# Performance work log

Measured on AMD Instinct MI355X. Metric: run time of the kernel, lower is better.

The kernel has to match this reference:

```python
import jax, jax.numpy as jnp
import numpy as np

N, C, K, NUM_CLASS = 400000, 128, 128, 128


def setup_inputs() -> dict:
    key = jax.random.key(0)
    k1, k2, k3 = jax.random.split(key, 3)
    outputs = jax.random.normal(k1, (N, C), dtype=jnp.float32)
    labels = jax.random.randint(k2, (N,), 0, 2 * NUM_CLASS, dtype=jnp.int64 if jax.config.read('jax_enable_x64') else jnp.int32)
    global_logit = jax.random.normal(k3, (K, C), dtype=jnp.float32)
    return {"outputs": outputs, "labels": labels, "global_logit": global_logit, "k": NUM_CLASS}


def _pairwise_dist(x, protos):
    # Euclidean distance ||proto_j - x_i|| for all (i, j) without a [N,K,C] temp.
    x2 = jnp.sum(x * x, axis=1, keepdims=True)            # [N,1]
    p2 = jnp.sum(protos * protos, axis=1)[None, :]        # [1,K]
    d2 = x2 + p2 - 2.0 * (x @ protos.T)                   # [N,K]
    return jnp.sqrt(jnp.maximum(d2, 0.0))


def reference(outputs, labels, global_logit, k):
    # Rows with labels <= k-1 keep their label; rows with labels > k-1 get the
    # nearest-prototype index. Since the concatenated (labeled + pseudo-labeled)
    # set covers every row and CE-mean is order-invariant, we compute per-row
    # effective labels and a single mean cross-entropy.
    dists = _pairwise_dist(outputs, global_logit)          # [N,K]
    min_dist_labels = jnp.argmin(dists, axis=1)            # [N]
    is_labeled = labels <= (k - 1)
    labels_eff = jnp.where(is_labeled, labels, min_dist_labels)
    logp = jax.nn.log_softmax(outputs, axis=-1)            # [N,C]
    nll = -jnp.take_along_axis(logp, labels_eff[:, None].astype(jnp.int32), axis=1)[:, 0]
    return jnp.mean(nll)
```

## Files before the change

kernel.cpp:

```cpp
#include <hip/hip_runtime.h>
#include <hip/hip_bf16.h>


#define C_DIM 128
#define TILE_ROWS 32
#define NTHREADS 256
#define XSTRIDE 136

typedef __bf16 bf16x8 __attribute__((ext_vector_type(8)));
typedef unsigned short ushort8 __attribute__((ext_vector_type(8)));
typedef float f32x4 __attribute__((ext_vector_type(4)));

union FragU { ushort8 u; bf16x8 b; };

__device__ __forceinline__ unsigned short f2bf(float f) {
    unsigned int u = __float_as_uint(f);
    u += 0x7fffu + ((u >> 16) & 1u);
    return (unsigned short)(u >> 16);
}
__device__ __forceinline__ float bf2f(unsigned short h) {
    return __uint_as_float(((unsigned int)h) << 16);
}

extern "C" __global__ void __launch_bounds__(NTHREADS)
ploss_main(const float* __restrict__ x, const int* __restrict__ labels,
           const float* __restrict__ protos, const int* __restrict__ kptr,
           float* __restrict__ accum, int n_tiles)
{
    __shared__ __attribute__((aligned(16))) unsigned short x_lds[TILE_ROWS * XSTRIDE];
    __shared__ float lse_lds[TILE_ROWS];
    __shared__ float wmin_s[4][TILE_ROWS];
    __shared__ int   wmin_j[4][TILE_ROWS];

    const int tid  = threadIdx.x;
    const int lane = tid & 63;
    const int wave = tid >> 6;
    const int l15  = lane & 15;
    const int quad = lane >> 4;
    const int kk   = kptr[0];

    FragU bfrag[2][4];
    float p2h[2];
#pragma unroll
    for (int nt = 0; nt < 2; ++nt) {
        const int j = wave * 32 + nt * 16 + l15;
        const float* pr = protos + j * C_DIM;
        float s = 0.f;
#pragma unroll
        for (int c = 0; c < 32; c += 4) {
            float4 v = *(const float4*)(pr + quad * 32 + c);
            s += v.x*v.x + v.y*v.y + v.z*v.z + v.w*v.w;
        }
        s += __shfl_xor(s, 16);
        s += __shfl_xor(s, 32);
        p2h[nt] = 0.5f * s;
#pragma unroll
        for (int kt = 0; kt < 4; ++kt) {
            const float* pp = pr + kt * 32 + quad * 8;
            float4 v0 = *(const float4*)(pp);
            float4 v1 = *(const float4*)(pp + 4);
            FragU f;
            f.u[0]=f2bf(v0.x); f.u[1]=f2bf(v0.y); f.u[2]=f2bf(v0.z); f.u[3]=f2bf(v0.w);
            f.u[4]=f2bf(v1.x); f.u[5]=f2bf(v1.y); f.u[6]=f2bf(v1.z); f.u[7]=f2bf(v1.w);
            bfrag[nt][kt] = f;
        }
    }

    const int row_r = tid >> 3;
    const int row_q = tid & 7;

    float nll_acc = 0.f;

    for (int tile = blockIdx.x; tile < n_tiles; tile += gridDim.x) {
        const long long row0 = (long long)tile * TILE_ROWS;
        __syncthreads();

        const float* xr = x + (row0 + row_r) * C_DIM + row_q * 16;
        float4 a0 = *(const float4*)(xr);
        float4 a1 = *(const float4*)(xr + 4);
        float4 a2 = *(const float4*)(xr + 8);
        float4 a3 = *(const float4*)(xr + 12);

        float m = fmaxf(fmaxf(fmaxf(a0.x,a0.y),fmaxf(a0.z,a0.w)),
                        fmaxf(fmaxf(a1.x,a1.y),fmaxf(a1.z,a1.w)));
        m = fmaxf(m, fmaxf(fmaxf(fmaxf(a2.x,a2.y),fmaxf(a2.z,a2.w)),
                           fmaxf(fmaxf(a3.x,a3.y),fmaxf(a3.z,a3.w))));
        float s = __expf(a0.x-m)+__expf(a0.y-m)+__expf(a0.z-m)+__expf(a0.w-m)
                + __expf(a1.x-m)+__expf(a1.y-m)+__expf(a1.z-m)+__expf(a1.w-m)
                + __expf(a2.x-m)+__expf(a2.y-m)+__expf(a2.z-m)+__expf(a2.w-m)
                + __expf(a3.x-m)+__expf(a3.y-m)+__expf(a3.z-m)+__expf(a3.w-m);
#pragma unroll
        for (int mask = 1; mask <= 4; mask <<= 1) {
            float mo = __shfl_xor(m, mask);
            float so = __shfl_xor(s, mask);
            float nm = fmaxf(m, mo);
            s = s * __expf(m - nm) + so * __expf(mo - nm);
            m = nm;
        }
        if (row_q == 0) lse_lds[row_r] = m + __logf(s);

        FragU w0, w1;
        w0.u[0]=f2bf(a0.x); w0.u[1]=f2bf(a0.y); w0.u[2]=f2bf(a0.z); w0.u[3]=f2bf(a0.w);
        w0.u[4]=f2bf(a1.x); w0.u[5]=f2bf(a1.y); w0.u[6]=f2bf(a1.z); w0.u[7]=f2bf(a1.w);
        w1.u[0]=f2bf(a2.x); w1.u[1]=f2bf(a2.y); w1.u[2]=f2bf(a2.z); w1.u[3]=f2bf(a2.w);
        w1.u[4]=f2bf(a3.x); w1.u[5]=f2bf(a3.y); w1.u[6]=f2bf(a3.z); w1.u[7]=f2bf(a3.w);
        ushort8* dst = (ushort8*)&x_lds[row_r * XSTRIDE + row_q * 16];
        dst[0] = w0.u;
        dst[1] = w1.u;

        __syncthreads();

        f32x4 acc[2][2];
        f32x4 zero = {0.f, 0.f, 0.f, 0.f};
        acc[0][0]=zero; acc[0][1]=zero; acc[1][0]=zero; acc[1][1]=zero;
#pragma unroll
        for (int kt = 0; kt < 4; ++kt) {
#pragma unroll
            for (int mt = 0; mt < 2; ++mt) {
                FragU af;
                af.u = *(const ushort8*)&x_lds[(mt*16 + l15) * XSTRIDE + kt*32 + quad*8];
                acc[mt][0] = __builtin_amdgcn_mfma_f32_16x16x32_bf16(af.b, bfrag[0][kt].b, acc[mt][0], 0, 0, 0);
                acc[mt][1] = __builtin_amdgcn_mfma_f32_16x16x32_bf16(af.b, bfrag[1][kt].b, acc[mt][1], 0, 0, 0);
            }
        }

#pragma unroll
        for (int mt = 0; mt < 2; ++mt) {
#pragma unroll
            for (int reg = 0; reg < 4; ++reg) {
                float s0 = p2h[0] - acc[mt][0][reg];
                float s1 = p2h[1] - acc[mt][1][reg];
                int j0 = wave*32 + l15, j1 = j0 + 16;
                float sm; int jm;
                if (s1 < s0) { sm = s1; jm = j1; } else { sm = s0; jm = j0; }
#pragma unroll
                for (int mask = 1; mask <= 8; mask <<= 1) {
                    float so = __shfl_xor(sm, mask);
                    int   jo = __shfl_xor(jm, mask);
                    if (so < sm || (so == sm && jo < jm)) { sm = so; jm = jo; }
                }
                if (l15 == 0) {
                    int r = mt*16 + quad*4 + reg;
                    wmin_s[wave][r] = sm;
                    wmin_j[wave][r] = jm;
                }
            }
        }
        __syncthreads();

        if (tid < TILE_ROWS) {
            float bs = wmin_s[0][tid]; int bj = wmin_j[0][tid];
#pragma unroll
            for (int w = 1; w < 4; ++w) {
                float s2 = wmin_s[w][tid]; int j2 = wmin_j[w][tid];
                if (s2 < bs) { bs = s2; bj = j2; }
            }
            int lab = labels[row0 + tid];
            int eff = (lab <= kk - 1) ? lab : bj;
            float xv = bf2f(x_lds[tid * XSTRIDE + eff]);
            nll_acc += lse_lds[tid] - xv;
        }
    }

    if (wave == 0) {
        float v = nll_acc;
#pragma unroll
        for (int mask = 32; mask >= 1; mask >>= 1) v += __shfl_xor(v, mask);
        if (lane == 0) atomicAdd(accum, v);
    }
}

extern "C" __global__ void ploss_finalize(const float* __restrict__ accum,
                                          float* __restrict__ out, float inv_n)
{
    out[0] = accum[0] * inv_n;
}

extern "C" void kernel_launch(void* const* d_in, const int* in_sizes, int n_in,
                              void* d_out, int out_size, void* d_ws, size_t ws_size,
                              hipStream_t stream)
{
    const float* x      = (const float*)d_in[0];
    const int*   labels = (const int*)d_in[1];
    const float* protos = (const float*)d_in[2];
    const int*   kptr   = (const int*)d_in[3];
    const int n_rows  = in_sizes[0] / C_DIM;
    const int n_tiles = n_rows / TILE_ROWS;

    float* accum = (float*)d_ws;
    hipMemsetAsync(accum, 0, sizeof(float), stream);

    int grid = 1024;
    if (grid > n_tiles) grid = n_tiles;
    ploss_main<<<grid, NTHREADS, 0, stream>>>(x, labels, protos, kptr, accum, n_tiles);
    ploss_finalize<<<1, 1, 0, stream>>>(accum, (float*)d_out, 1.0f / (float)n_rows);
}
```

Before: 357.7 us.

## Prefetch next tile into registers with double-buffered LDS and packed argmin keys

Restructures the tile loop to load the next tile's rows and labels into registers while the current tile is processed, and double-buffers the LDS tile so one barrier per iteration suffices. The distance/index argmin is packed into a single ordered unsigned key, halving shuffles and LDS traffic. Grid size is raised to 2048 blocks. This hides global load latency but raises register use, and truncating low distance bits can alter tie-breaking among near-equal prototypes.

```diff
diff --git a/kernel.cpp b/kernel.cpp
--- a/kernel.cpp
+++ b/kernel.cpp
@@ -6,6 +6,7 @@
 #define TILE_ROWS 32
 #define NTHREADS 256
 #define XSTRIDE 136
+#define GRID 2048
 
 typedef __bf16 bf16x8 __attribute__((ext_vector_type(8)));
 typedef unsigned short ushort8 __attribute__((ext_vector_type(8)));
@@ -20,6 +21,10 @@
 }
 __device__ __forceinline__ float bf2f(unsigned short h) {
     return __uint_as_float(((unsigned int)h) << 16);
+}
+__device__ __forceinline__ unsigned f2ord(float s) {
+    unsigned u = __float_as_uint(s);
+    return (u & 0x80000000u) ? ~u : (u | 0x80000000u);
 }
 
 extern "C" __global__ void __launch_bounds__(NTHREADS)
@@ -27,10 +32,9 @@
            const float* __restrict__ protos, const int* __restrict__ kptr,
            float* __restrict__ accum, int n_tiles)
 {
-    __shared__ __attribute__((aligned(16))) unsigned short x_lds[TILE_ROWS * XSTRIDE];
-    __shared__ float lse_lds[TILE_ROWS];
-    __shared__ float wmin_s[4][TILE_ROWS];
-    __shared__ int   wmin_j[4][TILE_ROWS];
+    __shared__ __attribute__((aligned(16))) unsigned short x_lds[2][TILE_ROWS * XSTRIDE];
+    __shared__ float lse_lds[2][TILE_ROWS];
+    __shared__ unsigned wmin_u[4][TILE_ROWS];
 
     const int tid  = threadIdx.x;
     const int lane = tid & 63;
@@ -70,16 +74,33 @@
     const int row_q = tid & 7;
 
     float nll_acc = 0.f;
-
-    for (int tile = blockIdx.x; tile < n_tiles; tile += gridDim.x) {
-        const long long row0 = (long long)tile * TILE_ROWS;
-        __syncthreads();
-
-        const float* xr = x + (row0 + row_r) * C_DIM + row_q * 16;
-        float4 a0 = *(const float4*)(xr);
-        float4 a1 = *(const float4*)(xr + 4);
-        float4 a2 = *(const float4*)(xr + 8);
-        float4 a3 = *(const float4*)(xr + 12);
+    int p = 0;
+
+    int t = blockIdx.x;
+    float4 a0, a1, a2, a3;
+    int lab = 0;
+    {
+        const float* xr = x + ((long long)t * TILE_ROWS + row_r) * C_DIM + row_q * 16;
+        a0 = *(const float4*)(xr);
+        a1 = *(const float4*)(xr + 4);
+        a2 = *(const float4*)(xr + 8);
+        a3 = *(const float4*)(xr + 12);
+        if (tid < TILE_ROWS) lab = labels[(long long)t * TILE_ROWS + tid];
+    }
+
+    for (; t < n_tiles; t += GRID) {
+        const int tn = t + GRID;
+        const int tl = (tn < n_tiles) ? tn : t;
+        float4 b0, b1, b2, b3;
+        int labn = 0;
+        {
+            const float* xr = x + ((long long)tl * TILE_ROWS + row_r) * C_DIM + row_q * 16;
+            b0 = *(const float4*)(xr);
+            b1 = *(const float4*)(xr + 4);
+            b2 = *(const float4*)(xr + 8);
+            b3 = *(const float4*)(xr + 12);
+            if (tid < TILE_ROWS) labn = labels[(long long)tl * TILE_ROWS + tid];
+        }
 
         float m = fmaxf(fmaxf(fmaxf(a0.x,a0.y),fmaxf(a0.z,a0.w)),
                         fmaxf(fmaxf(a1.x,a1.y),fmaxf(a1.z,a1.w)));
@@ -97,14 +118,14 @@
             s = s * __expf(m - nm) + so * __expf(mo - nm);
             m = nm;
         }
-        if (row_q == 0) lse_lds[row_r] = m + __logf(s);
+        if (row_q == 0) lse_lds[p][row_r] = m + __logf(s);
 
         FragU w0, w1;
         w0.u[0]=f2bf(a0.x); w0.u[1]=f2bf(a0.y); w0.u[2]=f2bf(a0.z); w0.u[3]=f2bf(a0.w);
         w0.u[4]=f2bf(a1.x); w0.u[5]=f2bf(a1.y); w0.u[6]=f2bf(a1.z); w0.u[7]=f2bf(a1.w);
         w1.u[0]=f2bf(a2.x); w1.u[1]=f2bf(a2.y); w1.u[2]=f2bf(a2.z); w1.u[3]=f2bf(a2.w);
         w1.u[4]=f2bf(a3.x); w1.u[5]=f2bf(a3.y); w1.u[6]=f2bf(a3.z); w1.u[7]=f2bf(a3.w);
-        ushort8* dst = (ushort8*)&x_lds[row_r * XSTRIDE + row_q * 16];
+        ushort8* dst = (ushort8*)&x_lds[p][row_r * XSTRIDE + row_q * 16];
         dst[0] = w0.u;
         dst[1] = w1.u;
 
@@ -118,48 +139,43 @@
 #pragma unroll
             for (int mt = 0; mt < 2; ++mt) {
                 FragU af;
-                af.u = *(const ushort8*)&x_lds[(mt*16 + l15) * XSTRIDE + kt*32 + quad*8];
+                af.u = *(const ushort8*)&x_lds[p][(mt*16 + l15) * XSTRIDE + kt*32 + quad*8];
                 acc[mt][0] = __builtin_amdgcn_mfma_f32_16x16x32_bf16(af.b, bfrag[0][kt].b, acc[mt][0], 0, 0, 0);
                 acc[mt][1] = __builtin_amdgcn_mfma_f32_16x16x32_bf16(af.b, bfrag[1][kt].b, acc[mt][1], 0, 0, 0);
             }
         }
 
+        const unsigned j0 = (unsigned)(wave*32 + l15);
 #pragma unroll
         for (int mt = 0; mt < 2; ++mt) {
 #pragma unroll
             for (int reg = 0; reg < 4; ++reg) {
-                float s0 = p2h[0] - acc[mt][0][reg];
-                float s1 = p2h[1] - acc[mt][1][reg];
-                int j0 = wave*32 + l15, j1 = j0 + 16;
-                float sm; int jm;
-                if (s1 < s0) { sm = s1; jm = j1; } else { sm = s0; jm = j0; }
+                unsigned u0 = (f2ord(p2h[0] - acc[mt][0][reg]) & 0xFFFFFF80u) | j0;
+                unsigned u1 = (f2ord(p2h[1] - acc[mt][1][reg]) & 0xFFFFFF80u) | (j0 + 16u);
+                unsigned u = u0 < u1 ? u0 : u1;
 #pragma unroll
                 for (int mask = 1; mask <= 8; mask <<= 1) {
-                    float so = __shfl_xor(sm, mask);
-                    int   jo = __shfl_xor(jm, mask);
-                    if (so < sm || (so == sm && jo < jm)) { sm = so; jm = jo; }
+                    unsigned uo = __shfl_xor(u, mask);
+                    u = uo < u ? uo : u;
                 }
-                if (l15 == 0) {
-                    int r = mt*16 + quad*4 + reg;
-                    wmin_s[wave][r] = sm;
-                    wmin_j[wave][r] = jm;
-                }
+                if (l15 == 0) wmin_u[wave][mt*16 + quad*4 + reg] = u;
             }
         }
         __syncthreads();
 
         if (tid < TILE_ROWS) {
-            float bs = wmin_s[0][tid]; int bj = wmin_j[0][tid];
-#pragma unroll
-            for (int w = 1; w < 4; ++w) {
-                float s2 = wmin_s[w][tid]; int j2 = wmin_j[w][tid];
-                if (s2 < bs) { bs = s2; bj = j2; }
-            }
-            int lab = labels[row0 + tid];
-            int eff = (lab <= kk - 1) ? lab : bj;
-            float xv = bf2f(x_lds[tid * XSTRIDE + eff]);
-            nll_acc += lse_lds[tid] - xv;
-        }
+            unsigned u = wmin_u[0][tid];
+            unsigned u1 = wmin_u[1][tid]; u = u1 < u ? u1 : u;
+            unsigned u2 = wmin_u[2][tid]; u = u2 < u ? u2 : u;
+            unsigned u3 = wmin_u[3][tid]; u = u3 < u ? u3 : u;
+            const int bj = (int)(u & 127u);
+            const int eff = (lab <= kk - 1) ? lab : bj;
+            const float xv = bf2f(x_lds[p][tid * XSTRIDE + eff]);
+            nll_acc += lse_lds[p][tid] - xv;
+        }
+
+        a0 = b0; a1 = b1; a2 = b2; a3 = b3; lab = labn;
+        p ^= 1;
     }
 
     if (wave == 0) {
@@ -190,7 +206,7 @@
     float* accum = (float*)d_ws;
     hipMemsetAsync(accum, 0, sizeof(float), stream);
 
-    int grid = 1024;
+    int grid = GRID;
     if (grid > n_tiles) grid = n_tiles;
     ploss_main<<<grid, NTHREADS, 0, stream>>>(x, labels, protos, kptr, accum, n_tiles);
     ploss_finalize<<<1, 1, 0, stream>>>(accum, (float*)d_out, 1.0f / (float)n_rows);
```

After: 309.6 us. -13.5%, faster.

## Give each wave whole row tiles with 32x32 MFMA and packed argmin

Applied to the files above, without the earlier changes.

Restructures the kernel so each wave owns entire 32-row tiles. A wave loads x straight into registers, computes the log-sum-exp with one cross-half shuffle, and runs 32x32x16 bf16 MFMAs against all 128 prototypes, whose fragments are staged once per block in LDS. The argmin packs the score and the index into one unsigned compare, with a bias on p2 so the scores stay positive, which removes the per-tile block barriers and the multi-stage shuffle argmin. It also launches many small blocks of 4 tiles per wave instead of a persistent grid, and reads the label logit back from global fp32. The cost is a per-block prototype setup, more registers, and truncated-score tie behaviour in the argmin.

```diff
diff --git a/kernel.cpp b/kernel.cpp
--- a/kernel.cpp
+++ b/kernel.cpp
@@ -5,21 +5,19 @@
 #define C_DIM 128
 #define TILE_ROWS 32
 #define NTHREADS 256
-#define XSTRIDE 136
+#define WAVES_PER_BLOCK 4
+#define TILES_PER_WAVE 4
 
 typedef __bf16 bf16x8 __attribute__((ext_vector_type(8)));
 typedef unsigned short ushort8 __attribute__((ext_vector_type(8)));
-typedef float f32x4 __attribute__((ext_vector_type(4)));
+typedef float f32x16 __attribute__((ext_vector_type(16)));
 
 union FragU { ushort8 u; bf16x8 b; };
 
 __device__ __forceinline__ unsigned short f2bf(float f) {
-    unsigned int u = __float_as_uint(f);
+    unsigned u = __float_as_uint(f);
     u += 0x7fffu + ((u >> 16) & 1u);
     return (unsigned short)(u >> 16);
-}
-__device__ __forceinline__ float bf2f(unsigned short h) {
-    return __uint_as_float(((unsigned int)h) << 16);
 }
 
 extern "C" __global__ void __launch_bounds__(NTHREADS)
@@ -27,147 +25,126 @@
            const float* __restrict__ protos, const int* __restrict__ kptr,
            float* __restrict__ accum, int n_tiles)
 {
-    __shared__ __attribute__((aligned(16))) unsigned short x_lds[TILE_ROWS * XSTRIDE];
-    __shared__ float lse_lds[TILE_ROWS];
-    __shared__ float wmin_s[4][TILE_ROWS];
-    __shared__ int   wmin_j[4][TILE_ROWS];
+    __shared__ __attribute__((aligned(16))) unsigned short pfrag[32 * 64 * 8];
+    __shared__ __attribute__((aligned(16))) float p2_lds[C_DIM];
 
     const int tid  = threadIdx.x;
     const int lane = tid & 63;
     const int wave = tid >> 6;
-    const int l15  = lane & 15;
-    const int quad = lane >> 4;
+    const int h    = lane >> 5;
+    const int m    = lane & 31;
     const int kk   = kptr[0];
 
-    FragU bfrag[2][4];
-    float p2h[2];
-#pragma unroll
-    for (int nt = 0; nt < 2; ++nt) {
-        const int j = wave * 32 + nt * 16 + l15;
-        const float* pr = protos + j * C_DIM;
+    if (tid < C_DIM) {
+        const float* pr = protos + tid * C_DIM;
         float s = 0.f;
 #pragma unroll
-        for (int c = 0; c < 32; c += 4) {
-            float4 v = *(const float4*)(pr + quad * 32 + c);
+        for (int c = 0; c < C_DIM; c += 4) {
+            float4 v = *(const float4*)(pr + c);
             s += v.x*v.x + v.y*v.y + v.z*v.z + v.w*v.w;
         }
-        s += __shfl_xor(s, 16);
-        s += __shfl_xor(s, 32);
-        p2h[nt] = 0.5f * s;
+        p2_lds[tid] = 0.5f * s + 512.0f;
+    }
+
+    {
+        const int pt = wave;
 #pragma unroll
-        for (int kt = 0; kt < 4; ++kt) {
-            const float* pp = pr + kt * 32 + quad * 8;
+        for (int kt = 0; kt < 8; ++kt) {
+            const float* pp = protos + (pt*32 + m) * C_DIM + kt*16 + h*8;
             float4 v0 = *(const float4*)(pp);
             float4 v1 = *(const float4*)(pp + 4);
             FragU f;
             f.u[0]=f2bf(v0.x); f.u[1]=f2bf(v0.y); f.u[2]=f2bf(v0.z); f.u[3]=f2bf(v0.w);
             f.u[4]=f2bf(v1.x); f.u[5]=f2bf(v1.y); f.u[6]=f2bf(v1.z); f.u[7]=f2bf(v1.w);
-            bfrag[nt][kt] = f;
+            *(ushort8*)&pfrag[((pt*8 + kt)*64 + lane)*8] = f.u;
+        }
+    }
+    __syncthreads();
+
+    const int gw = blockIdx.x * WAVES_PER_BLOCK + wave;
+    int t0 = gw * TILES_PER_WAVE;
+    int t1 = t0 + TILES_PER_WAVE;
+    if (t1 > n_tiles) t1 = n_tiles;
+
+    float nll = 0.f;
+
+#pragma unroll 1
+    for (int t = t0; t < t1; ++t) {
+        const float* xr = x + (size_t)(t * TILE_ROWS + m) * C_DIM + h * 8;
+        float4 v[16];
+#pragma unroll
+        for (int kt = 0; kt < 8; ++kt) {
+            v[2*kt]   = *(const float4*)(xr + kt*16);
+            v[2*kt+1] = *(const float4*)(xr + kt*16 + 4);
+        }
+        const int lab = labels[t * TILE_ROWS + m];
+
+        float mx = -3.4e38f;
+#pragma unroll
+        for (int i = 0; i < 16; ++i)
+            mx = fmaxf(mx, fmaxf(fmaxf(v[i].x, v[i].y), fmaxf(v[i].z, v[i].w)));
+        mx = fmaxf(mx, __shfl_xor(mx, 32));
+        float s = 0.f;
+#pragma unroll
+        for (int i = 0; i < 16; ++i)
+            s += __expf(v[i].x-mx) + __expf(v[i].y-mx) + __expf(v[i].z-mx) + __expf(v[i].w-mx);
+        s += __shfl_xor(s, 32);
+        const float lse = mx + __logf(s);
+
+        FragU xb[8];
+#pragma unroll
+        for (int kt = 0; kt < 8; ++kt) {
+            xb[kt].u[0]=f2bf(v[2*kt].x);   xb[kt].u[1]=f2bf(v[2*kt].y);
+            xb[kt].u[2]=f2bf(v[2*kt].z);   xb[kt].u[3]=f2bf(v[2*kt].w);
+            xb[kt].u[4]=f2bf(v[2*kt+1].x); xb[kt].u[5]=f2bf(v[2*kt+1].y);
+            xb[kt].u[6]=f2bf(v[2*kt+1].z); xb[kt].u[7]=f2bf(v[2*kt+1].w);
+        }
+
+        f32x16 acc[4];
+#pragma unroll
+        for (int pt = 0; pt < 4; ++pt) acc[pt] = (f32x16)(0.f);
+#pragma unroll
+        for (int kt = 0; kt < 8; ++kt) {
+#pragma unroll
+            for (int pt = 0; pt < 4; ++pt) {
+                FragU af;
+                af.u = *(const ushort8*)&pfrag[((pt*8 + kt)*64 + lane)*8];
+                acc[pt] = __builtin_amdgcn_mfma_f32_32x32x16_bf16(af.b, xb[kt].b, acc[pt], 0, 0, 0);
+            }
+        }
+
+        unsigned best = 0xFFFFFFFFu;
+#pragma unroll
+        for (int pt = 0; pt < 4; ++pt) {
+#pragma unroll
+            for (int g = 0; g < 4; ++g) {
+                float4 q = *(const float4*)&p2_lds[pt*32 + g*8 + h*4];
+#pragma unroll
+                for (int c = 0; c < 4; ++c) {
+                    const int r = g*4 + c;
+                    const float sc = q[c] - acc[pt][r];
+                    const unsigned j = (unsigned)(pt*32 + g*8 + h*4 + c);
+                    const unsigned u = (__float_as_uint(sc) & 0xFFFFFF80u) | j;
+                    best = u < best ? u : best;
+                }
+            }
+        }
+        {
+            const unsigned ub = __shfl_xor(best, 32);
+            best = ub < best ? ub : best;
+        }
+
+        if (lane < 32) {
+            const int bj  = (int)(best & 127u);
+            const int eff = (lab <= kk - 1) ? lab : bj;
+            const float xv = x[(size_t)(t * TILE_ROWS + m) * C_DIM + eff];
+            nll += lse - xv;
         }
     }
 
-    const int row_r = tid >> 3;
-    const int row_q = tid & 7;
-
-    float nll_acc = 0.f;
-
-    for (int tile = blockIdx.x; tile < n_tiles; tile += gridDim.x) {
-        const long long row0 = (long long)tile * TILE_ROWS;
-        __syncthreads();
-
-        const float* xr = x + (row0 + row_r) * C_DIM + row_q * 16;
-        float4 a0 = *(const float4*)(xr);
-        float4 a1 = *(const float4*)(xr + 4);
-        float4 a2 = *(const float4*)(xr + 8);
-        float4 a3 = *(const float4*)(xr + 12);
-
-        float m = fmaxf(fmaxf(fmaxf(a0.x,a0.y),fmaxf(a0.z,a0.w)),
-                        fmaxf(fmaxf(a1.x,a1.y),fmaxf(a1.z,a1.w)));
-        m = fmaxf(m, fmaxf(fmaxf(fmaxf(a2.x,a2.y),fmaxf(a2.z,a2.w)),
-                           fmaxf(fmaxf(a3.x,a3.y),fmaxf(a3.z,a3.w))));
-        float s = __expf(a0.x-m)+__expf(a0.y-m)+__expf(a0.z-m)+__expf(a0.w-m)
-                + __expf(a1.x-m)+__expf(a1.y-m)+__expf(a1.z-m)+__expf(a1.w-m)
-                + __expf(a2.x-m)+__expf(a2.y-m)+__expf(a2.z-m)+__expf(a2.w-m)
-                + __expf(a3.x-m)+__expf(a3.y-m)+__expf(a3.z-m)+__expf(a3.w-m);
 #pragma unroll
-        for (int mask = 1; mask <= 4; mask <<= 1) {
-            float mo = __shfl_xor(m, mask);
-            float so = __shfl_xor(s, mask);
-            float nm = fmaxf(m, mo);
-            s = s * __expf(m - nm) + so * __expf(mo - nm);
-            m = nm;
-        }
-        if (row_q == 0) lse_lds[row_r] = m + __logf(s);
-
-        FragU w0, w1;
-        w0.u[0]=f2bf(a0.x); w0.u[1]=f2bf(a0.y); w0.u[2]=f2bf(a0.z); w0.u[3]=f2bf(a0.w);
-        w0.u[4]=f2bf(a1.x); w0.u[5]=f2bf(a1.y); w0.u[6]=f2bf(a1.z); w0.u[7]=f2bf(a1.w);
-        w1.u[0]=f2bf(a2.x); w1.u[1]=f2bf(a2.y); w1.u[2]=f2bf(a2.z); w1.u[3]=f2bf(a2.w);
-        w1.u[4]=f2bf(a3.x); w1.u[5]=f2bf(a3.y); w1.u[6]=f2bf(a3.z); w1.u[7]=f2bf(a3.w);
-        ushort8* dst = (ushort8*)&x_lds[row_r * XSTRIDE + row_q * 16];
-        dst[0] = w0.u;
-        dst[1] = w1.u;
-
-        __syncthreads();
-
-        f32x4 acc[2][2];
-        f32x4 zero = {0.f, 0.f, 0.f, 0.f};
-        acc[0][0]=zero; acc[0][1]=zero; acc[1][0]=zero; acc[1][1]=zero;
-#pragma unroll
-        for (int kt = 0; kt < 4; ++kt) {
-#pragma unroll
-            for (int mt = 0; mt < 2; ++mt) {
-                FragU af;
-                af.u = *(const ushort8*)&x_lds[(mt*16 + l15) * XSTRIDE + kt*32 + quad*8];
-                acc[mt][0] = __builtin_amdgcn_mfma_f32_16x16x32_bf16(af.b, bfrag[0][kt].b, acc[mt][0], 0, 0, 0);
-                acc[mt][1] = __builtin_amdgcn_mfma_f32_16x16x32_bf16(af.b, bfrag[1][kt].b, acc[mt][1], 0, 0, 0);
-            }
-        }
-
-#pragma unroll
-        for (int mt = 0; mt < 2; ++mt) {
-#pragma unroll
-            for (int reg = 0; reg < 4; ++reg) {
-                float s0 = p2h[0] - acc[mt][0][reg];
-                float s1 = p2h[1] - acc[mt][1][reg];
-                int j0 = wave*32 + l15, j1 = j0 + 16;
-                float sm; int jm;
-                if (s1 < s0) { sm = s1; jm = j1; } else { sm = s0; jm = j0; }
-#pragma unroll
-                for (int mask = 1; mask <= 8; mask <<= 1) {
-                    float so = __shfl_xor(sm, mask);
-                    int   jo = __shfl_xor(jm, mask);
-                    if (so < sm || (so == sm && jo < jm)) { sm = so; jm = jo; }
-                }
-                if (l15 == 0) {
-                    int r = mt*16 + quad*4 + reg;
-                    wmin_s[wave][r] = sm;
-                    wmin_j[wave][r] = jm;
-                }
-            }
-        }
-        __syncthreads();
-
-        if (tid < TILE_ROWS) {
-            float bs = wmin_s[0][tid]; int bj = wmin_j[0][tid];
-#pragma unroll
-            for (int w = 1; w < 4; ++w) {
-                float s2 = wmin_s[w][tid]; int j2 = wmin_j[w][tid];
-                if (s2 < bs) { bs = s2; bj = j2; }
-            }
-            int lab = labels[row0 + tid];
-            int eff = (lab <= kk - 1) ? lab : bj;
-            float xv = bf2f(x_lds[tid * XSTRIDE + eff]);
-            nll_acc += lse_lds[tid] - xv;
-        }
-    }
-
-    if (wave == 0) {
-        float v = nll_acc;
-#pragma unroll
-        for (int mask = 32; mask >= 1; mask >>= 1) v += __shfl_xor(v, mask);
-        if (lane == 0) atomicAdd(accum, v);
-    }
+    for (int mask = 1; mask <= 32; mask <<= 1) nll += __shfl_xor(nll, mask);
+    if (lane == 0) atomicAdd(accum, nll);
 }
 
 extern "C" __global__ void ploss_finalize(const float* __restrict__ accum,
@@ -190,8 +167,8 @@
     float* accum = (float*)d_ws;
     hipMemsetAsync(accum, 0, sizeof(float), stream);
 
-    int grid = 1024;
-    if (grid > n_tiles) grid = n_tiles;
+    const int grid = (n_tiles + WAVES_PER_BLOCK * TILES_PER_WAVE - 1)
+                   / (WAVES_PER_BLOCK * TILES_PER_WAVE);
     ploss_main<<<grid, NTHREADS, 0, stream>>>(x, labels, protos, kptr, accum, n_tiles);
     ploss_finalize<<<1, 1, 0, stream>>>(accum, (float*)d_out, 1.0f / (float)n_rows);
 }
```

Result: faster. 344.9 us (-3.6%).
